# Kernel optimization log

Hardware: AMD Instinct MI355X
Metric: run time of the kernel (lower is better)

Reference implementation:

```python
import jax, jax.numpy as jnp
import numpy as np

INPUT_SIZE = 64
HIDDEN_SIZE = 256


def setup_inputs() -> dict:
    key = jax.random.key(0)
    ks = jax.random.split(key, 20)
    I, H = INPUT_SIZE, HIDDEN_SIZE
    s = 0.05
    inp = {
        "x": jax.random.normal(ks[0], (256, 512, I), jnp.float32),
        # LSTM params (PyTorch layout: [4H, in], gate order i,f,g,o)
        "w_ih": jax.random.normal(ks[1], (4 * H, I), jnp.float32) * s,
        "w_hh": jax.random.normal(ks[2], (4 * H, H), jnp.float32) * s,
        "b_ih": jax.random.normal(ks[3], (4 * H,), jnp.float32) * s,
        "b_hh": jax.random.normal(ks[4], (4 * H,), jnp.float32) * s,
        # fc_pit: H -> 64 -> 1
        "pit_w1": jax.random.normal(ks[5], (64, H), jnp.float32) * s,
        "pit_b1": jax.random.normal(ks[6], (64,), jnp.float32) * s,
        "pit_w2": jax.random.normal(ks[7], (1, 64), jnp.float32) * s,
        "pit_b2": jax.random.normal(ks[8], (1,), jnp.float32) * s,
        # fc_time: H+1 -> 64 -> 1
        "time_w1": jax.random.normal(ks[9], (64, H + 1), jnp.float32) * s,
        "time_b1": jax.random.normal(ks[10], (64,), jnp.float32) * s,
        "time_w2": jax.random.normal(ks[11], (1, 64), jnp.float32) * s,
        "time_b2": jax.random.normal(ks[12], (1,), jnp.float32) * s,
        "ar_w1": jax.random.normal(ks[13], (64, I + 2), jnp.float32) * s,
        "ar_b1": jax.random.normal(ks[14], (64,), jnp.float32) * s,
        "ar_w2": jax.random.normal(ks[15], (I, 64), jnp.float32) * s,
        "ar_b2": jax.random.normal(ks[16], (I,), jnp.float32) * s,
    }
    return inp


def _forward(x, w_ih, w_hh, b_ih, b_hh, pit_w1, pit_b1, pit_w2, pit_b2,
             time_w1, time_b1, time_w2, time_b2, ar_w1, ar_b1, ar_w2, ar_b2):
    B, S, I = x.shape
    H = w_hh.shape[1]

    def step(carry, x_orig_t):
        x_t, h, c = carry  # x_t: [B, I], h/c: [B, H]
        gates = x_t @ w_ih.T + b_ih + h @ w_hh.T + b_hh  # [B, 4H]
        i_g, f_g, g_g, o_g = jnp.split(gates, 4, axis=-1)
        i_g = jax.nn.sigmoid(i_g)
        f_g = jax.nn.sigmoid(f_g)
        g_g = jnp.tanh(g_g)
        o_g = jax.nn.sigmoid(o_g)
        c = f_g * c + i_g * g_g
        h = o_g * jnp.tanh(c)
        pit = jax.nn.relu(h @ pit_w1.T + pit_b1) @ pit_w2.T + pit_b2  # [B, 1]
        t_in = jnp.concatenate([h, pit], axis=1)  # [B, H+1]
        time = jax.nn.relu(t_in @ time_w1.T + time_b1) @ time_w2.T + time_b2  # [B, 1]
        ar_in = jnp.concatenate([pit, time, x_orig_t], axis=-1)  # [B, I+2]
        nxt = jax.nn.relu(ar_in @ ar_w1.T + ar_b1) @ ar_w2.T + ar_b2  # [B, I]
        return (nxt, h, c), (pit[:, 0], time[:, 0], nxt)

    h0 = jnp.zeros((B, H), x.dtype)
    c0 = jnp.zeros((B, H), x.dtype)
    x0 = x[:, 0, :]
    x_sbI = jnp.swapaxes(x, 0, 1)  # [S, B, I] original inputs fed at each step
    _, (pits, times, nxts) = jax.lax.scan(step, (x0, h0, c0), x_sbI)
    pit_pred = pits.T  # [B, S]
    time_pred = times.T  # [B, S]
    ar_out = jnp.concatenate([x[:, :1, :], jnp.swapaxes(nxts, 0, 1)[:, : S - 1, :]], axis=1)
    return pit_pred, time_pred, ar_out


def reference(x, w_ih, w_hh, b_ih, b_hh, pit_w1, pit_b1, pit_w2, pit_b2,
              time_w1, time_b1, time_w2, time_b2, ar_w1, ar_b1, ar_w2, ar_b2):
    return _forward(x, w_ih, w_hh, b_ih, b_hh, pit_w1, pit_b1, pit_w2, pit_b2,
                    time_w1, time_b1, time_w2, time_b2, ar_w1, ar_b1, ar_w2, ar_b2)
```

## Files before the change

kernel.cpp:

```cpp
#include <hip/hip_runtime.h>
#include <hip/hip_bf16.h>
#include <hip/hip_fp8.h>


typedef float f32x4 __attribute__((ext_vector_type(4)));
typedef short s16x8 __attribute__((ext_vector_type(8)));

#define S_LEN 512
#define I_DIM 64
#define NT    512

#define WSB_G8   0
#define WSTRIDE8 40960
#define WSB_BF   327680
#define PREP_N   368640

#define OUT_PIT  0
#define OUT_TIME 131072
#define OUT_AR   262144

#define ALD 328
#define AF8 336
#define XLD 72

__device__ __forceinline__ float sigf(float x) {
  return 1.0f / (1.0f + __expf(-x));
}
__device__ __forceinline__ float tanh_fast(float x) {
  float c = fminf(fmaxf(x, -15.0f), 15.0f);
  float e = __expf(2.0f * c);
  return (e - 1.0f) / (e + 1.0f);
}
__device__ __forceinline__ unsigned short f2bf(float f) {
  __hip_bfloat16 h = __float2bfloat16(f);
  return *reinterpret_cast<unsigned short*>(&h);
}
__device__ __forceinline__ unsigned char f2f8(float v) {
  __hip_fp8_e4m3 q(v);
  return *reinterpret_cast<unsigned char*>(&q);
}
__device__ __forceinline__ void sync_lds() {
  asm volatile("s_waitcnt lgkmcnt(0)" ::: "memory");
  __builtin_amdgcn_s_barrier();
  asm volatile("" ::: "memory");
}
__device__ __forceinline__ void gld16(const void* g, void* l) {
  __builtin_amdgcn_global_load_lds(
      (const __attribute__((address_space(1))) unsigned int*)g,
      (__attribute__((address_space(3))) unsigned int*)l, 16, 0, 0);
}

__global__ void prep_kernel(const float* __restrict__ w_ih,
                            const float* __restrict__ w_hh,
                            const float* __restrict__ pit_w1,
                            const float* __restrict__ time_w1,
                            const float* __restrict__ ar_w1,
                            const float* __restrict__ ar_w2,
                            unsigned char* __restrict__ ws8) {
  int idx = blockIdx.x * 256 + threadIdx.x;
  if (idx >= PREP_N) return;
  if (idx < WSB_G8 + 327680) {
    int w  = idx / WSTRIDE8;
    int p8 = idx - w * WSTRIDE8;
    int f  = p8 >> 9;
    int b  = p8 & 511;
    int lane = b >> 3, e = b & 7;
    int lrow = lane & 15, lgrp = lane >> 4;
    int ktidx = f >> 3, qm = f & 7;
    int kt = (ktidx < 8) ? ktidx + 2 : ktidx - 8;
    int row = (qm >> 1) * 256 + w * 32 + (qm & 1) * 16 + lrow;
    int col = kt * 32 + lgrp * 8 + e;
    float v = (col < I_DIM) ? w_ih[row * I_DIM + col]
                            : w_hh[row * 256 + col - I_DIM];
    ws8[idx] = f2f8(v);
  } else {
    int e2 = idx - 327680;
    int lane = (e2 >> 3) & 63;
    int e    = e2 & 7;
    int lrow = lane & 15, lgrp = lane >> 4;
    float v;
    if (e2 < 16384) {
      int f = e2 >> 9, wv = f >> 3, kt = f & 7;
      v = pit_w1[(wv * 16 + lrow) * 256 + kt * 32 + lgrp * 8 + e];
    } else if (e2 < 32768) {
      int f = (e2 - 16384) >> 9, wv = f >> 3, kt = f & 7;
      v = time_w1[(wv * 16 + lrow) * 257 + kt * 32 + lgrp * 8 + e];
    } else if (e2 < 36864) {
      int f = (e2 - 32768) >> 9, wv = f >> 1, kt = f & 1;
      v = ar_w1[(wv * 16 + lrow) * 66 + 2 + kt * 32 + lgrp * 8 + e];
    } else {
      int f = (e2 - 36864) >> 9, wv = f >> 1, kt = f & 1;
      v = ar_w2[(wv * 16 + lrow) * 64 + kt * 32 + lgrp * 8 + e];
    }
    ((unsigned short*)(ws8 + WSB_BF))[e2] = f2bf(v);
  }
}

#define A8FRAG(kt) (*(const long*)&A_f8[lrow][(kt) * 32 + 8 * lgrp])

#define DMA4F(ktidx, slot)                                                     \
  do {                                                                         \
    const unsigned char* g_ = wg8l + (ktidx) * 4096;                           \
    gld16(g_,        &stg8[wave][slot][0]);                                    \
    gld16(g_ + 1024, &stg8[wave][slot][1024]);                                 \
    gld16(g_ + 2048, &stg8[wave][slot][2048]);                                 \
    gld16(g_ + 3072, &stg8[wave][slot][3072]);                                 \
  } while (0)

#define GCHUNK8(af, slot)                                                      \
  do {                                                                         \
    asm volatile("s_waitcnt vmcnt(4)" ::: "memory");                           \
    _Pragma("unroll")                                                          \
    for (int s_ = 0; s_ < 8; ++s_) {                                           \
      long b_ = *(const long*)&stg8[wave][slot][s_ * 512 + lane * 8];          \
      acc2[s_] = __builtin_amdgcn_mfma_f32_16x16x32_fp8_fp8(                   \
          (af), b_, acc2[s_], 0, 0, 0);                                        \
    }                                                                          \
    asm volatile("s_waitcnt lgkmcnt(0)" ::: "memory");                         \
  } while (0)

__global__ __launch_bounds__(NT, 2) void rnn_kernel(
    const float* __restrict__ x,
    const float* __restrict__ b_ih, const float* __restrict__ b_hh,
    const float* __restrict__ pit_b1, const float* __restrict__ pit_w2,
    const float* __restrict__ pit_b2,
    const float* __restrict__ time_w1, const float* __restrict__ time_b1,
    const float* __restrict__ time_w2, const float* __restrict__ time_b2,
    const float* __restrict__ ar_w1, const float* __restrict__ ar_b1,
    const float* __restrict__ ar_b2,
    const unsigned char* __restrict__ ws8,
    float* __restrict__ out)
{
  __shared__ __align__(16) unsigned short A_lds[16][ALD];
  __shared__ __align__(16) unsigned char  A_f8[16][AF8];
  __shared__ __align__(16) unsigned short xo_lds[16][XLD];
  __shared__ __align__(16) unsigned short ar1_lds[16][XLD];
  __shared__ __align__(16) unsigned short pit_lds[32 * 512];
  __shared__ __align__(16) unsigned short tim_lds[32 * 512];
  __shared__ __align__(16) unsigned char  stg8[8][2][4096];
  __shared__ float pitp[4][16];
  __shared__ float timep[4][16];

  const int tid  = threadIdx.x;
  const int wave = tid >> 6;
  const int lane = tid & 63;
  const int lrow = lane & 15;
  const int lgrp = lane >> 4;
  const int b0   = blockIdx.x * 16;
  const int hcol = (wave & 3) * 16 + lrow;
  const unsigned char* wg8l = ws8 + wave * WSTRIDE8 + lane * 16;
  const unsigned char* wg8  = ws8 + wave * WSTRIDE8;
  const unsigned short* wsb = (const unsigned short*)(ws8 + WSB_BF);

  for (int c = tid; c < 2048; c += NT) {
    *(s16x8*)&pit_lds[c * 8] = *(const s16x8*)&wsb[c * 8];
    *(s16x8*)&tim_lds[c * 8] = *(const s16x8*)&wsb[16384 + c * 8];
  }
  for (int i = tid; i < 16 * ALD; i += NT) (&A_lds[0][0])[i] = 0;

  float gbias[8];
#pragma unroll
  for (int qm = 0; qm < 8; ++qm) {
    int g = (qm >> 1) * 256 + wave * 32 + (qm & 1) * 16 + lrow;
    gbias[qm] = b_ih[g] + b_hh[g];
  }
  s16x8 arw[2];
  float pb1v = 0, pw2v = 0, tb1v = 0, tw2v = 0, twlv = 0;
  float ab1v = 0, arpv = 0, artv = 0, ab2v = 0;
  if (wave < 4) {
    arw[0] = *(const s16x8*)&wsb[32768 + ((wave & 3) * 2 + 0) * 512 + lane * 8];
    arw[1] = *(const s16x8*)&wsb[32768 + ((wave & 3) * 2 + 1) * 512 + lane * 8];
    pb1v = pit_b1[hcol]; pw2v = pit_w2[hcol];
    ab1v = ar_b1[hcol];  arpv = ar_w1[hcol * 66]; artv = ar_w1[hcol * 66 + 1];
  } else {
    arw[0] = *(const s16x8*)&wsb[36864 + ((wave & 3) * 2 + 0) * 512 + lane * 8];
    arw[1] = *(const s16x8*)&wsb[36864 + ((wave & 3) * 2 + 1) * 512 + lane * 8];
    tb1v = time_b1[hcol]; tw2v = time_w2[hcol];
    twlv = time_w1[hcol * 257 + 256]; ab2v = ar_b2[hcol];
  }
  const float pb2 = pit_b2[0], tb2 = time_b2[0];

  const int srow = tid >> 5;
  const int sc2  = (tid & 31) * 2;
  const size_t xbase = (size_t)(b0 + srow) * S_LEN * I_DIM + sc2;
  float2 xpre = *reinterpret_cast<const float2*>(&x[xbase]);
  __syncthreads();
  A_lds[srow][sc2]     = f2bf(xpre.x);
  A_lds[srow][sc2 + 1] = f2bf(xpre.y);
  A_f8[srow][sc2]      = f2f8(xpre.x);
  A_f8[srow][sc2 + 1]  = f2f8(xpre.y);
  *reinterpret_cast<float2*>(&out[OUT_AR + xbase]) = xpre;

  float cst[2][4];
#pragma unroll
  for (int m = 0; m < 2; ++m)
#pragma unroll
    for (int r = 0; r < 4; ++r) cst[m][r] = 0.0f;
  __syncthreads();

  f32x4 acc2[8];
#pragma unroll
  for (int qm = 0; qm < 8; ++qm) {
    f32x4 tv; tv[0] = tv[1] = tv[2] = tv[3] = gbias[qm];
    acc2[qm] = tv;
  }
  {
    long a0 = A8FRAG(0);
#pragma unroll
    for (int qm = 0; qm < 8; ++qm) {
      long b = *(const long*)(wg8 + (64 + qm) * 512 + lane * 8);
      acc2[qm] = __builtin_amdgcn_mfma_f32_16x16x32_fp8_fp8(a0, b, acc2[qm], 0, 0, 0);
    }
    long a1 = A8FRAG(1);
#pragma unroll
    for (int qm = 0; qm < 8; ++qm) {
      long b = *(const long*)(wg8 + (72 + qm) * 512 + lane * 8);
      acc2[qm] = __builtin_amdgcn_mfma_f32_16x16x32_fp8_fp8(a1, b, acc2[qm], 0, 0, 0);
    }
  }
  asm volatile("s_waitcnt vmcnt(0)" ::: "memory");
  DMA4F(0, 0);
  DMA4F(1, 1);

  for (int t = 0; t < S_LEN; ++t) {
    xo_lds[srow][sc2]     = f2bf(xpre.x);
    xo_lds[srow][sc2 + 1] = f2bf(xpre.y);
    if (t + 1 < S_LEN)
      xpre = *reinterpret_cast<const float2*>(&x[xbase + (size_t)(t + 1) * I_DIM]);

#pragma unroll
    for (int m = 0; m < 2; ++m)
#pragma unroll
      for (int r = 0; r < 4; ++r) {
        float ig = sigf(acc2[0 + m][r]);
        float fg = sigf(acc2[2 + m][r]);
        float gg = tanh_fast(acc2[4 + m][r]);
        float og = sigf(acc2[6 + m][r]);
        float c  = fg * cst[m][r] + ig * gg;
        cst[m][r] = c;
        float hv = og * tanh_fast(c);
        int row = lgrp * 4 + r, col = 64 + wave * 32 + m * 16 + lrow;
        A_lds[row][col] = f2bf(hv);
        A_f8[row][col]  = f2f8(hv);
      }
#pragma unroll
    for (int qm = 0; qm < 8; ++qm) {
      f32x4 tv; tv[0] = tv[1] = tv[2] = tv[3] = gbias[qm];
      acc2[qm] = tv;
    }
    sync_lds();

    s16x8 hfr[8];
    long  hfr8[8];
#pragma unroll
    for (int k = 0; k < 8; ++k) {
      hfr[k]  = *(const s16x8*)&A_lds[lrow][64 + k * 32 + 8 * lgrp];
      hfr8[k] = *(const long*)&A_f8[lrow][64 + k * 32 + 8 * lgrp];
    }
    f32x4 hacc;
    {
      float hb = (wave < 4) ? pb1v : tb1v;
      hacc[0] = hacc[1] = hacc[2] = hacc[3] = hb;
      const unsigned short* hbp = (wave < 4) ? pit_lds : tim_lds;
#pragma unroll
      for (int kt = 0; kt < 8; ++kt) {
        s16x8 bH = *(const s16x8*)&hbp[(((wave & 3) * 8 + kt) * 64 + lane) * 8];
        hacc = __builtin_amdgcn_mfma_f32_16x16x32_bf16(hfr[kt], bH, hacc, 0, 0, 0);
      }
    }
    if (wave < 4) {
      float v[4];
#pragma unroll
      for (int r = 0; r < 4; ++r) v[r] = fmaxf(hacc[r], 0.0f) * pw2v;
#pragma unroll
      for (int off = 1; off < 16; off <<= 1)
#pragma unroll
        for (int r = 0; r < 4; ++r) v[r] += __shfl_xor(v[r], off);
      if (lrow == 0) {
#pragma unroll
        for (int r = 0; r < 4; ++r) pitp[wave][lgrp * 4 + r] = v[r];
      }
    }
    GCHUNK8(hfr8[0], 0); DMA4F(2, 0);
    GCHUNK8(hfr8[1], 1); DMA4F(3, 1);
    GCHUNK8(hfr8[2], 0); DMA4F(4, 0);
    GCHUNK8(hfr8[3], 1); DMA4F(5, 1);
    sync_lds();

    float pv[4];
#pragma unroll
    for (int r = 0; r < 4; ++r) {
      int row = lgrp * 4 + r;
      pv[r] = pitp[0][row] + pitp[1][row] + pitp[2][row] + pitp[3][row] + pb2;
    }
    f32x4 aracc;
    if (wave < 4) {
      aracc[0] = aracc[1] = aracc[2] = aracc[3] = ab1v;
#pragma unroll
      for (int kt = 0; kt < 2; ++kt) {
        s16x8 aX = *(const s16x8*)&xo_lds[lrow][kt * 32 + 8 * lgrp];
        aracc = __builtin_amdgcn_mfma_f32_16x16x32_bf16(aX, arw[kt], aracc, 0, 0, 0);
      }
      if (wave == 0 && lane < 16) {
        float pvs = pitp[0][lane] + pitp[1][lane] + pitp[2][lane] + pitp[3][lane] + pb2;
        out[OUT_PIT + (size_t)(b0 + lane) * S_LEN + t] = pvs;
      }
    } else {
      float v[4];
#pragma unroll
      for (int r = 0; r < 4; ++r)
        v[r] = fmaxf(hacc[r] + pv[r] * twlv, 0.0f) * tw2v;
#pragma unroll
      for (int off = 1; off < 16; off <<= 1)
#pragma unroll
        for (int r = 0; r < 4; ++r) v[r] += __shfl_xor(v[r], off);
      if (lrow == 0) {
#pragma unroll
        for (int r = 0; r < 4; ++r) timep[wave & 3][lgrp * 4 + r] = v[r];
      }
    }
    GCHUNK8(hfr8[4], 0); DMA4F(6, 0);
    GCHUNK8(hfr8[5], 1); DMA4F(7, 1);
    sync_lds();

    float tvv[4];
#pragma unroll
    for (int r = 0; r < 4; ++r) {
      int row = lgrp * 4 + r;
      tvv[r] = timep[0][row] + timep[1][row] + timep[2][row] + timep[3][row] + tb2;
    }
    if (wave < 4) {
#pragma unroll
      for (int r = 0; r < 4; ++r) {
        float a1 = aracc[r] + pv[r] * arpv + tvv[r] * artv;
        ar1_lds[lgrp * 4 + r][hcol] = f2bf(fmaxf(a1, 0.0f));
      }
    } else if (wave == 4 && lane < 16) {
      float tvs = timep[0][lane] + timep[1][lane] + timep[2][lane] + timep[3][lane] + tb2;
      out[OUT_TIME + (size_t)(b0 + lane) * S_LEN + t] = tvs;
    }
    GCHUNK8(hfr8[6], 0); DMA4F(8, 0);
    GCHUNK8(hfr8[7], 1); DMA4F(9, 1);
    sync_lds();

    if (wave >= 4) {
      f32x4 nacc;
      nacc[0] = nacc[1] = nacc[2] = nacc[3] = ab2v;
#pragma unroll
      for (int kt = 0; kt < 2; ++kt) {
        s16x8 aR = *(const s16x8*)&ar1_lds[lrow][kt * 32 + 8 * lgrp];
        nacc = __builtin_amdgcn_mfma_f32_16x16x32_bf16(aR, arw[kt], nacc, 0, 0, 0);
      }
#pragma unroll
      for (int r = 0; r < 4; ++r) {
        int row = lgrp * 4 + r;
        float nv = nacc[r];
        A_lds[row][hcol] = f2bf(nv);
        A_f8[row][hcol]  = f2f8(nv);
        if (t < S_LEN - 1)
          out[OUT_AR + (size_t)(b0 + row) * S_LEN * I_DIM + (size_t)(t + 1) * I_DIM + hcol] = nv;
      }
    }
    sync_lds();

    {
      long a0 = A8FRAG(0);
      GCHUNK8(a0, 0); DMA4F(0, 0);
      long a1 = A8FRAG(1);
      GCHUNK8(a1, 1); DMA4F(1, 1);
    }
  }
}

extern "C" void kernel_launch(void* const* d_in, const int* in_sizes, int n_in,
                              void* d_out, int out_size, void* d_ws, size_t ws_size,
                              hipStream_t stream) {
  const float* x       = (const float*)d_in[0];
  const float* w_ih    = (const float*)d_in[1];
  const float* w_hh    = (const float*)d_in[2];
  const float* b_ih    = (const float*)d_in[3];
  const float* b_hh    = (const float*)d_in[4];
  const float* pit_w1  = (const float*)d_in[5];
  const float* pit_b1  = (const float*)d_in[6];
  const float* pit_w2  = (const float*)d_in[7];
  const float* pit_b2  = (const float*)d_in[8];
  const float* time_w1 = (const float*)d_in[9];
  const float* time_b1 = (const float*)d_in[10];
  const float* time_w2 = (const float*)d_in[11];
  const float* time_b2 = (const float*)d_in[12];
  const float* ar_w1   = (const float*)d_in[13];
  const float* ar_b1   = (const float*)d_in[14];
  const float* ar_w2   = (const float*)d_in[15];
  const float* ar_b2   = (const float*)d_in[16];
  unsigned char* ws8   = (unsigned char*)d_ws;
  float* out           = (float*)d_out;

  prep_kernel<<<dim3((PREP_N + 255) / 256), dim3(256), 0, stream>>>(
      w_ih, w_hh, pit_w1, time_w1, ar_w1, ar_w2, ws8);
  rnn_kernel<<<dim3(16), dim3(NT), 0, stream>>>(
      x, b_ih, b_hh, pit_b1, pit_w2, pit_b2,
      time_w1, time_b1, time_w2, time_b2,
      ar_w1, ar_b1, ar_b2, ws8, out);
}
```

Measured before the change: 3.490 ms.

## Stream FC head weights as fp8 via triple-buffered DMA pipeline instead of bf16 LDS

The pit/time first-layer head weights move from bf16 copies resident in LDS to fp8 chunks stored per wave in the workspace, streamed through the same global-to-LDS DMA pipeline as the LSTM gate weights. The staging buffer grows from double to triple buffering, with adjusted vmcnt waits and a reworked half-chunk schedule for the x-input part. The bf16 copy of the activation matrix is dropped, so only the fp8 copy is written. This frees a large amount of LDS and removes bf16 stores, in exchange for more global traffic per step and lower precision in the head matmul.

Measured after the change: 3.796 ms. +8.8%, slower.

```diff
diff --git a/kernel.cpp b/kernel.cpp
--- a/kernel.cpp
+++ b/kernel.cpp
@@ -10,16 +10,14 @@
 #define I_DIM 64
 #define NT    512
 
-#define WSB_G8   0
-#define WSTRIDE8 40960
-#define WSB_BF   327680
+#define WSTRIDE8 45056
+#define WSB_BF   360448
 #define PREP_N   368640
 
 #define OUT_PIT  0
 #define OUT_TIME 131072
 #define OUT_AR   262144
 
-#define ALD 328
 #define AF8 336
 #define XLD 72
 
@@ -59,37 +57,38 @@
                             unsigned char* __restrict__ ws8) {
   int idx = blockIdx.x * 256 + threadIdx.x;
   if (idx >= PREP_N) return;
-  if (idx < WSB_G8 + 327680) {
+  if (idx < WSB_BF) {
     int w  = idx / WSTRIDE8;
     int p8 = idx - w * WSTRIDE8;
     int f  = p8 >> 9;
     int b  = p8 & 511;
     int lane = b >> 3, e = b & 7;
     int lrow = lane & 15, lgrp = lane >> 4;
-    int ktidx = f >> 3, qm = f & 7;
-    int kt = (ktidx < 8) ? ktidx + 2 : ktidx - 8;
-    int row = (qm >> 1) * 256 + w * 32 + (qm & 1) * 16 + lrow;
-    int col = kt * 32 + lgrp * 8 + e;
-    float v = (col < I_DIM) ? w_ih[row * I_DIM + col]
-                            : w_hh[row * 256 + col - I_DIM];
+    float v;
+    if (f < 8) {
+      int row = (w & 3) * 16 + lrow;
+      int col = f * 32 + lgrp * 8 + e;
+      v = (w < 4) ? pit_w1[row * 256 + col] : time_w1[row * 257 + col];
+    } else {
+      int g = f - 8;
+      int ktidx = g >> 3, qm = g & 7;
+      int kt = (ktidx < 8) ? ktidx + 2 : ktidx - 8;
+      int row = (qm >> 1) * 256 + w * 32 + (qm & 1) * 16 + lrow;
+      int col = kt * 32 + lgrp * 8 + e;
+      v = (col < I_DIM) ? w_ih[row * I_DIM + col] : w_hh[row * 256 + col - I_DIM];
+    }
     ws8[idx] = f2f8(v);
   } else {
-    int e2 = idx - 327680;
+    int e2 = idx - WSB_BF;
     int lane = (e2 >> 3) & 63;
     int e    = e2 & 7;
     int lrow = lane & 15, lgrp = lane >> 4;
     float v;
-    if (e2 < 16384) {
-      int f = e2 >> 9, wv = f >> 3, kt = f & 7;
-      v = pit_w1[(wv * 16 + lrow) * 256 + kt * 32 + lgrp * 8 + e];
-    } else if (e2 < 32768) {
-      int f = (e2 - 16384) >> 9, wv = f >> 3, kt = f & 7;
-      v = time_w1[(wv * 16 + lrow) * 257 + kt * 32 + lgrp * 8 + e];
-    } else if (e2 < 36864) {
-      int f = (e2 - 32768) >> 9, wv = f >> 1, kt = f & 1;
+    if (e2 < 4096) {
+      int f = e2 >> 9, wv = f >> 1, kt = f & 1;
       v = ar_w1[(wv * 16 + lrow) * 66 + 2 + kt * 32 + lgrp * 8 + e];
     } else {
-      int f = (e2 - 36864) >> 9, wv = f >> 1, kt = f & 1;
+      int f = (e2 - 4096) >> 9, wv = f >> 1, kt = f & 1;
       v = ar_w2[(wv * 16 + lrow) * 64 + kt * 32 + lgrp * 8 + e];
     }
     ((unsigned short*)(ws8 + WSB_BF))[e2] = f2bf(v);
@@ -98,23 +97,51 @@
 
 #define A8FRAG(kt) (*(const long*)&A_f8[lrow][(kt) * 32 + 8 * lgrp])
 
-#define DMA4F(ktidx, slot)                                                     \
+#define DMA4F(byteoff, slot)                                                   \
   do {                                                                         \
-    const unsigned char* g_ = wg8l + (ktidx) * 4096;                           \
+    const unsigned char* g_ = wg8l + (byteoff);                                \
     gld16(g_,        &stg8[wave][slot][0]);                                    \
     gld16(g_ + 1024, &stg8[wave][slot][1024]);                                 \
     gld16(g_ + 2048, &stg8[wave][slot][2048]);                                 \
     gld16(g_ + 3072, &stg8[wave][slot][3072]);                                 \
   } while (0)
-
-#define GCHUNK8(af, slot)                                                      \
+#define DMA2F(byteoff, slot)                                                   \
   do {                                                                         \
-    asm volatile("s_waitcnt vmcnt(4)" ::: "memory");                           \
+    const unsigned char* g_ = wg8l + (byteoff);                                \
+    gld16(g_,        &stg8[wave][slot][0]);                                    \
+    gld16(g_ + 1024, &stg8[wave][slot][1024]);                                 \
+  } while (0)
+
+#define CHEADF(slot, N)                                                        \
+  do {                                                                         \
+    asm volatile("s_waitcnt vmcnt(" #N ")" ::: "memory");                      \
+    _Pragma("unroll")                                                          \
+    for (int k_ = 0; k_ < 8; ++k_) {                                           \
+      long b_ = *(const long*)&stg8[wave][slot][k_ * 512 + lane * 8];          \
+      hacc = __builtin_amdgcn_mfma_f32_16x16x32_fp8_fp8(hfr8[k_], b_,          \
+                                                        hacc, 0, 0, 0);        \
+    }                                                                          \
+    asm volatile("s_waitcnt lgkmcnt(0)" ::: "memory");                         \
+  } while (0)
+#define GCHUNK8(af, slot, N)                                                   \
+  do {                                                                         \
+    asm volatile("s_waitcnt vmcnt(" #N ")" ::: "memory");                      \
     _Pragma("unroll")                                                          \
     for (int s_ = 0; s_ < 8; ++s_) {                                           \
       long b_ = *(const long*)&stg8[wave][slot][s_ * 512 + lane * 8];          \
       acc2[s_] = __builtin_amdgcn_mfma_f32_16x16x32_fp8_fp8(                   \
           (af), b_, acc2[s_], 0, 0, 0);                                        \
+    }                                                                          \
+    asm volatile("s_waitcnt lgkmcnt(0)" ::: "memory");                         \
+  } while (0)
+#define GHALF4(af, slot, N, qb)                                                \
+  do {                                                                         \
+    asm volatile("s_waitcnt vmcnt(" #N ")" ::: "memory");                      \
+    _Pragma("unroll")                                                          \
+    for (int s_ = 0; s_ < 4; ++s_) {                                           \
+      long b_ = *(const long*)&stg8[wave][slot][s_ * 512 + lane * 8];          \
+      acc2[(qb) + s_] = __builtin_amdgcn_mfma_f32_16x16x32_fp8_fp8(            \
+          (af), b_, acc2[(qb) + s_], 0, 0, 0);                                 \
     }                                                                          \
     asm volatile("s_waitcnt lgkmcnt(0)" ::: "memory");                         \
   } while (0)
@@ -131,13 +158,10 @@
     const unsigned char* __restrict__ ws8,
     float* __restrict__ out)
 {
-  __shared__ __align__(16) unsigned short A_lds[16][ALD];
   __shared__ __align__(16) unsigned char  A_f8[16][AF8];
   __shared__ __align__(16) unsigned short xo_lds[16][XLD];
   __shared__ __align__(16) unsigned short ar1_lds[16][XLD];
-  __shared__ __align__(16) unsigned short pit_lds[32 * 512];
-  __shared__ __align__(16) unsigned short tim_lds[32 * 512];
-  __shared__ __align__(16) unsigned char  stg8[8][2][4096];
+  __shared__ __align__(16) unsigned char  stg8[8][3][4096];
   __shared__ float pitp[4][16];
   __shared__ float timep[4][16];
 
@@ -152,11 +176,7 @@
   const unsigned char* wg8  = ws8 + wave * WSTRIDE8;
   const unsigned short* wsb = (const unsigned short*)(ws8 + WSB_BF);
 
-  for (int c = tid; c < 2048; c += NT) {
-    *(s16x8*)&pit_lds[c * 8] = *(const s16x8*)&wsb[c * 8];
-    *(s16x8*)&tim_lds[c * 8] = *(const s16x8*)&wsb[16384 + c * 8];
-  }
-  for (int i = tid; i < 16 * ALD; i += NT) (&A_lds[0][0])[i] = 0;
+  for (int i = tid; i < 16 * AF8; i += NT) (&A_f8[0][0])[i] = 0;
 
   float gbias[8];
 #pragma unroll
@@ -168,13 +188,13 @@
   float pb1v = 0, pw2v = 0, tb1v = 0, tw2v = 0, twlv = 0;
   float ab1v = 0, arpv = 0, artv = 0, ab2v = 0;
   if (wave < 4) {
-    arw[0] = *(const s16x8*)&wsb[32768 + ((wave & 3) * 2 + 0) * 512 + lane * 8];
-    arw[1] = *(const s16x8*)&wsb[32768 + ((wave & 3) * 2 + 1) * 512 + lane * 8];
+    arw[0] = *(const s16x8*)&wsb[((wave & 3) * 2 + 0) * 512 + lane * 8];
+    arw[1] = *(const s16x8*)&wsb[((wave & 3) * 2 + 1) * 512 + lane * 8];
     pb1v = pit_b1[hcol]; pw2v = pit_w2[hcol];
     ab1v = ar_b1[hcol];  arpv = ar_w1[hcol * 66]; artv = ar_w1[hcol * 66 + 1];
   } else {
-    arw[0] = *(const s16x8*)&wsb[36864 + ((wave & 3) * 2 + 0) * 512 + lane * 8];
-    arw[1] = *(const s16x8*)&wsb[36864 + ((wave & 3) * 2 + 1) * 512 + lane * 8];
+    arw[0] = *(const s16x8*)&wsb[4096 + ((wave & 3) * 2 + 0) * 512 + lane * 8];
+    arw[1] = *(const s16x8*)&wsb[4096 + ((wave & 3) * 2 + 1) * 512 + lane * 8];
     tb1v = time_b1[hcol]; tw2v = time_w2[hcol];
     twlv = time_w1[hcol * 257 + 256]; ab2v = ar_b2[hcol];
   }
@@ -185,10 +205,8 @@
   const size_t xbase = (size_t)(b0 + srow) * S_LEN * I_DIM + sc2;
   float2 xpre = *reinterpret_cast<const float2*>(&x[xbase]);
   __syncthreads();
-  A_lds[srow][sc2]     = f2bf(xpre.x);
-  A_lds[srow][sc2 + 1] = f2bf(xpre.y);
-  A_f8[srow][sc2]      = f2f8(xpre.x);
-  A_f8[srow][sc2 + 1]  = f2f8(xpre.y);
+  A_f8[srow][sc2]     = f2f8(xpre.x);
+  A_f8[srow][sc2 + 1] = f2f8(xpre.y);
   *reinterpret_cast<float2*>(&out[OUT_AR + xbase]) = xpre;
 
   float cst[2][4];
@@ -208,19 +226,20 @@
     long a0 = A8FRAG(0);
 #pragma unroll
     for (int qm = 0; qm < 8; ++qm) {
-      long b = *(const long*)(wg8 + (64 + qm) * 512 + lane * 8);
+      long b = *(const long*)(wg8 + 36864 + qm * 512 + lane * 8);
       acc2[qm] = __builtin_amdgcn_mfma_f32_16x16x32_fp8_fp8(a0, b, acc2[qm], 0, 0, 0);
     }
     long a1 = A8FRAG(1);
 #pragma unroll
     for (int qm = 0; qm < 8; ++qm) {
-      long b = *(const long*)(wg8 + (72 + qm) * 512 + lane * 8);
+      long b = *(const long*)(wg8 + 40960 + qm * 512 + lane * 8);
       acc2[qm] = __builtin_amdgcn_mfma_f32_16x16x32_fp8_fp8(a1, b, acc2[qm], 0, 0, 0);
     }
   }
   asm volatile("s_waitcnt vmcnt(0)" ::: "memory");
   DMA4F(0, 0);
-  DMA4F(1, 1);
+  DMA4F(4096, 1);
+  DMA4F(8192, 2);
 
   for (int t = 0; t < S_LEN; ++t) {
     xo_lds[srow][sc2]     = f2bf(xpre.x);
@@ -238,10 +257,7 @@
         float og = sigf(acc2[6 + m][r]);
         float c  = fg * cst[m][r] + ig * gg;
         cst[m][r] = c;
-        float hv = og * tanh_fast(c);
-        int row = lgrp * 4 + r, col = 64 + wave * 32 + m * 16 + lrow;
-        A_lds[row][col] = f2bf(hv);
-        A_f8[row][col]  = f2f8(hv);
+        A_f8[lgrp * 4 + r][64 + wave * 32 + m * 16 + lrow] = f2f8(og * tanh_fast(c));
       }
 #pragma unroll
     for (int qm = 0; qm < 8; ++qm) {
@@ -250,24 +266,20 @@
     }
     sync_lds();
 
-    s16x8 hfr[8];
-    long  hfr8[8];
-#pragma unroll
-    for (int k = 0; k < 8; ++k) {
-      hfr[k]  = *(const s16x8*)&A_lds[lrow][64 + k * 32 + 8 * lgrp];
+    long hfr8[8];
+#pragma unroll
+    for (int k = 0; k < 8; ++k)
       hfr8[k] = *(const long*)&A_f8[lrow][64 + k * 32 + 8 * lgrp];
-    }
+
     f32x4 hacc;
     {
       float hb = (wave < 4) ? pb1v : tb1v;
       hacc[0] = hacc[1] = hacc[2] = hacc[3] = hb;
-      const unsigned short* hbp = (wave < 4) ? pit_lds : tim_lds;
-#pragma unroll
-      for (int kt = 0; kt < 8; ++kt) {
-        s16x8 bH = *(const s16x8*)&hbp[(((wave & 3) * 8 + kt) * 64 + lane) * 8];
-        hacc = __builtin_amdgcn_mfma_f32_16x16x32_bf16(hfr[kt], bH, hacc, 0, 0, 0);
-      }
-    }
+    }
+    CHEADF(0, 8);            DMA4F(12288, 0);
+    GCHUNK8(hfr8[0], 1, 8);  DMA4F(16384, 1);
+    GCHUNK8(hfr8[1], 2, 8);  DMA4F(20480, 2);
+
     if (wave < 4) {
       float v[4];
 #pragma unroll
@@ -281,10 +293,8 @@
         for (int r = 0; r < 4; ++r) pitp[wave][lgrp * 4 + r] = v[r];
       }
     }
-    GCHUNK8(hfr8[0], 0); DMA4F(2, 0);
-    GCHUNK8(hfr8[1], 1); DMA4F(3, 1);
-    GCHUNK8(hfr8[2], 0); DMA4F(4, 0);
-    GCHUNK8(hfr8[3], 1); DMA4F(5, 1);
+    GCHUNK8(hfr8[2], 0, 8);  DMA4F(24576, 0);
+    GCHUNK8(hfr8[3], 1, 8);  DMA4F(28672, 1);
     sync_lds();
 
     float pv[4];
@@ -319,8 +329,8 @@
         for (int r = 0; r < 4; ++r) timep[wave & 3][lgrp * 4 + r] = v[r];
       }
     }
-    GCHUNK8(hfr8[4], 0); DMA4F(6, 0);
-    GCHUNK8(hfr8[5], 1); DMA4F(7, 1);
+    GCHUNK8(hfr8[4], 2, 8);  DMA4F(32768, 2);
+    GCHUNK8(hfr8[5], 0, 8);  DMA4F(36864, 0);
     sync_lds();
 
     float tvv[4];
@@ -339,8 +349,8 @@
       float tvs = timep[0][lane] + timep[1][lane] + timep[2][lane] + timep[3][lane] + tb2;
       out[OUT_TIME + (size_t)(b0 + lane) * S_LEN + t] = tvs;
     }
-    GCHUNK8(hfr8[6], 0); DMA4F(8, 0);
-    GCHUNK8(hfr8[7], 1); DMA4F(9, 1);
+    GCHUNK8(hfr8[6], 1, 8);  DMA2F(40960, 1);
+    GCHUNK8(hfr8[7], 2, 6);  DMA2F(43008, 2);
     sync_lds();
 
     if (wave >= 4) {
@@ -355,8 +365,7 @@
       for (int r = 0; r < 4; ++r) {
         int row = lgrp * 4 + r;
         float nv = nacc[r];
-        A_lds[row][hcol] = f2bf(nv);
-        A_f8[row][hcol]  = f2f8(nv);
+        A_f8[row][hcol] = f2f8(nv);
         if (t < S_LEN - 1)
           out[OUT_AR + (size_t)(b0 + row) * S_LEN * I_DIM + (size_t)(t + 1) * I_DIM + hcol] = nv;
       }
@@ -365,9 +374,10 @@
 
     {
       long a0 = A8FRAG(0);
-      GCHUNK8(a0, 0); DMA4F(0, 0);
+      GCHUNK8(a0, 0, 4);     DMA4F(0, 0);
       long a1 = A8FRAG(1);
-      GCHUNK8(a1, 1); DMA4F(1, 1);
+      GHALF4(a1, 1, 6, 0);   DMA4F(4096, 1);
+      GHALF4(a1, 2, 8, 4);   DMA4F(8192, 2);
     }
   }
 }
```

## Double workgroup to 16 waves, split gate columns and head roles across waves

Applied to the files above, without the earlier changes.

Raises the block from 8 to 16 waves so that each wave owns 16 hidden columns (4 gate accumulators) instead of 32, halving the per-wave fp8 weight streaming and MFMA chain on the recurrent critical path. The pit, time, AR-first-layer and AR-second-layer heads are now assigned to disjoint groups of four waves rather than sharing waves. Launch bounds drop from 2 blocks per CU to 1, and the per-step barriers now synchronise twice as many waves, which costs occupancy and adds sync overhead.

After: 4.549 ms. +30.3%, slower.

```diff
diff --git a/kernel.cpp b/kernel.cpp
--- a/kernel.cpp
+++ b/kernel.cpp
@@ -8,10 +8,9 @@
 
 #define S_LEN 512
 #define I_DIM 64
-#define NT    512
-
-#define WSB_G8   0
-#define WSTRIDE8 40960
+#define NT    1024
+
+#define WSTRIDE8 20480
 #define WSB_BF   327680
 #define PREP_N   368640
 
@@ -59,22 +58,22 @@
                             unsigned char* __restrict__ ws8) {
   int idx = blockIdx.x * 256 + threadIdx.x;
   if (idx >= PREP_N) return;
-  if (idx < WSB_G8 + 327680) {
+  if (idx < WSB_BF) {
     int w  = idx / WSTRIDE8;
     int p8 = idx - w * WSTRIDE8;
     int f  = p8 >> 9;
     int b  = p8 & 511;
     int lane = b >> 3, e = b & 7;
     int lrow = lane & 15, lgrp = lane >> 4;
-    int ktidx = f >> 3, qm = f & 7;
+    int ktidx = f >> 2, q = f & 3;
     int kt = (ktidx < 8) ? ktidx + 2 : ktidx - 8;
-    int row = (qm >> 1) * 256 + w * 32 + (qm & 1) * 16 + lrow;
+    int row = q * 256 + w * 16 + lrow;
     int col = kt * 32 + lgrp * 8 + e;
     float v = (col < I_DIM) ? w_ih[row * I_DIM + col]
                             : w_hh[row * 256 + col - I_DIM];
     ws8[idx] = f2f8(v);
   } else {
-    int e2 = idx - 327680;
+    int e2 = idx - WSB_BF;
     int lane = (e2 >> 3) & 63;
     int e    = e2 & 7;
     int lrow = lane & 15, lgrp = lane >> 4;
@@ -98,28 +97,26 @@
 
 #define A8FRAG(kt) (*(const long*)&A_f8[lrow][(kt) * 32 + 8 * lgrp])
 
-#define DMA4F(ktidx, slot)                                                     \
+#define DMAC(byteoff, slot)                                                    \
   do {                                                                         \
-    const unsigned char* g_ = wg8l + (ktidx) * 4096;                           \
+    const unsigned char* g_ = wg8l + (byteoff);                                \
     gld16(g_,        &stg8[wave][slot][0]);                                    \
     gld16(g_ + 1024, &stg8[wave][slot][1024]);                                 \
-    gld16(g_ + 2048, &stg8[wave][slot][2048]);                                 \
-    gld16(g_ + 3072, &stg8[wave][slot][3072]);                                 \
   } while (0)
 
-#define GCHUNK8(af, slot)                                                      \
+#define GCHUNK(af, slot)                                                       \
   do {                                                                         \
-    asm volatile("s_waitcnt vmcnt(4)" ::: "memory");                           \
+    asm volatile("s_waitcnt vmcnt(2)" ::: "memory");                           \
     _Pragma("unroll")                                                          \
-    for (int s_ = 0; s_ < 8; ++s_) {                                           \
-      long b_ = *(const long*)&stg8[wave][slot][s_ * 512 + lane * 8];          \
-      acc2[s_] = __builtin_amdgcn_mfma_f32_16x16x32_fp8_fp8(                   \
-          (af), b_, acc2[s_], 0, 0, 0);                                        \
+    for (int q_ = 0; q_ < 4; ++q_) {                                           \
+      long b_ = *(const long*)&stg8[wave][slot][q_ * 512 + lane * 8];          \
+      acc2[q_] = __builtin_amdgcn_mfma_f32_16x16x32_fp8_fp8(                   \
+          (af), b_, acc2[q_], 0, 0, 0);                                        \
     }                                                                          \
     asm volatile("s_waitcnt lgkmcnt(0)" ::: "memory");                         \
   } while (0)
 
-__global__ __launch_bounds__(NT, 2) void rnn_kernel(
+__global__ __launch_bounds__(NT, 1) void rnn_kernel(
     const float* __restrict__ x,
     const float* __restrict__ b_ih, const float* __restrict__ b_hh,
     const float* __restrict__ pit_b1, const float* __restrict__ pit_w2,
@@ -137,7 +134,7 @@
   __shared__ __align__(16) unsigned short ar1_lds[16][XLD];
   __shared__ __align__(16) unsigned short pit_lds[32 * 512];
   __shared__ __align__(16) unsigned short tim_lds[32 * 512];
-  __shared__ __align__(16) unsigned char  stg8[8][2][4096];
+  __shared__ __align__(16) unsigned char  stg8[16][2][2048];
   __shared__ float pitp[4][16];
   __shared__ float timep[4][16];
 
@@ -157,115 +154,114 @@
     *(s16x8*)&tim_lds[c * 8] = *(const s16x8*)&wsb[16384 + c * 8];
   }
   for (int i = tid; i < 16 * ALD; i += NT) (&A_lds[0][0])[i] = 0;
-
-  float gbias[8];
-#pragma unroll
-  for (int qm = 0; qm < 8; ++qm) {
-    int g = (qm >> 1) * 256 + wave * 32 + (qm & 1) * 16 + lrow;
-    gbias[qm] = b_ih[g] + b_hh[g];
-  }
+  for (int i = tid; i < 16 * AF8; i += NT) (&A_f8[0][0])[i] = 0;
+
+  float gbias[4];
+#pragma unroll
+  for (int q = 0; q < 4; ++q)
+    gbias[q] = b_ih[q * 256 + wave * 16 + lrow] + b_hh[q * 256 + wave * 16 + lrow];
+
   s16x8 arw[2];
   float pb1v = 0, pw2v = 0, tb1v = 0, tw2v = 0, twlv = 0;
   float ab1v = 0, arpv = 0, artv = 0, ab2v = 0;
   if (wave < 4) {
+    pb1v = pit_b1[hcol]; pw2v = pit_w2[hcol];
+  } else if (wave < 8) {
+    tb1v = time_b1[hcol]; tw2v = time_w2[hcol];
+    twlv = time_w1[hcol * 257 + 256];
+  } else if (wave < 12) {
     arw[0] = *(const s16x8*)&wsb[32768 + ((wave & 3) * 2 + 0) * 512 + lane * 8];
     arw[1] = *(const s16x8*)&wsb[32768 + ((wave & 3) * 2 + 1) * 512 + lane * 8];
-    pb1v = pit_b1[hcol]; pw2v = pit_w2[hcol];
-    ab1v = ar_b1[hcol];  arpv = ar_w1[hcol * 66]; artv = ar_w1[hcol * 66 + 1];
+    ab1v = ar_b1[hcol]; arpv = ar_w1[hcol * 66]; artv = ar_w1[hcol * 66 + 1];
   } else {
     arw[0] = *(const s16x8*)&wsb[36864 + ((wave & 3) * 2 + 0) * 512 + lane * 8];
     arw[1] = *(const s16x8*)&wsb[36864 + ((wave & 3) * 2 + 1) * 512 + lane * 8];
-    tb1v = time_b1[hcol]; tw2v = time_w2[hcol];
-    twlv = time_w1[hcol * 257 + 256]; ab2v = ar_b2[hcol];
+    ab2v = ar_b2[hcol];
   }
   const float pb2 = pit_b2[0], tb2 = time_b2[0];
 
-  const int srow = tid >> 5;
-  const int sc2  = (tid & 31) * 2;
-  const size_t xbase = (size_t)(b0 + srow) * S_LEN * I_DIM + sc2;
-  float2 xpre = *reinterpret_cast<const float2*>(&x[xbase]);
+  const int srow = tid >> 6;
+  const int scol = tid & 63;
+  const size_t xbase = (size_t)(b0 + srow) * S_LEN * I_DIM + scol;
+  float xpre = x[xbase];
   __syncthreads();
-  A_lds[srow][sc2]     = f2bf(xpre.x);
-  A_lds[srow][sc2 + 1] = f2bf(xpre.y);
-  A_f8[srow][sc2]      = f2f8(xpre.x);
-  A_f8[srow][sc2 + 1]  = f2f8(xpre.y);
-  *reinterpret_cast<float2*>(&out[OUT_AR + xbase]) = xpre;
-
-  float cst[2][4];
-#pragma unroll
-  for (int m = 0; m < 2; ++m)
-#pragma unroll
-    for (int r = 0; r < 4; ++r) cst[m][r] = 0.0f;
+  A_lds[srow][scol] = f2bf(xpre);
+  A_f8[srow][scol]  = f2f8(xpre);
+  out[OUT_AR + xbase] = xpre;
+
+  float cst[4] = {0.0f, 0.0f, 0.0f, 0.0f};
   __syncthreads();
 
-  f32x4 acc2[8];
-#pragma unroll
-  for (int qm = 0; qm < 8; ++qm) {
-    f32x4 tv; tv[0] = tv[1] = tv[2] = tv[3] = gbias[qm];
-    acc2[qm] = tv;
+  f32x4 acc2[4];
+#pragma unroll
+  for (int q = 0; q < 4; ++q) {
+    f32x4 tv; tv[0] = tv[1] = tv[2] = tv[3] = gbias[q];
+    acc2[q] = tv;
   }
   {
     long a0 = A8FRAG(0);
 #pragma unroll
-    for (int qm = 0; qm < 8; ++qm) {
-      long b = *(const long*)(wg8 + (64 + qm) * 512 + lane * 8);
-      acc2[qm] = __builtin_amdgcn_mfma_f32_16x16x32_fp8_fp8(a0, b, acc2[qm], 0, 0, 0);
+    for (int q = 0; q < 4; ++q) {
+      long b = *(const long*)(wg8 + (32 + q) * 512 + lane * 8);
+      acc2[q] = __builtin_amdgcn_mfma_f32_16x16x32_fp8_fp8(a0, b, acc2[q], 0, 0, 0);
     }
     long a1 = A8FRAG(1);
 #pragma unroll
-    for (int qm = 0; qm < 8; ++qm) {
-      long b = *(const long*)(wg8 + (72 + qm) * 512 + lane * 8);
-      acc2[qm] = __builtin_amdgcn_mfma_f32_16x16x32_fp8_fp8(a1, b, acc2[qm], 0, 0, 0);
+    for (int q = 0; q < 4; ++q) {
+      long b = *(const long*)(wg8 + (36 + q) * 512 + lane * 8);
+      acc2[q] = __builtin_amdgcn_mfma_f32_16x16x32_fp8_fp8(a1, b, acc2[q], 0, 0, 0);
     }
   }
   asm volatile("s_waitcnt vmcnt(0)" ::: "memory");
-  DMA4F(0, 0);
-  DMA4F(1, 1);
+  DMAC(0, 0);
+  DMAC(2048, 1);
 
   for (int t = 0; t < S_LEN; ++t) {
-    xo_lds[srow][sc2]     = f2bf(xpre.x);
-    xo_lds[srow][sc2 + 1] = f2bf(xpre.y);
-    if (t + 1 < S_LEN)
-      xpre = *reinterpret_cast<const float2*>(&x[xbase + (size_t)(t + 1) * I_DIM]);
-
-#pragma unroll
-    for (int m = 0; m < 2; ++m)
-#pragma unroll
-      for (int r = 0; r < 4; ++r) {
-        float ig = sigf(acc2[0 + m][r]);
-        float fg = sigf(acc2[2 + m][r]);
-        float gg = tanh_fast(acc2[4 + m][r]);
-        float og = sigf(acc2[6 + m][r]);
-        float c  = fg * cst[m][r] + ig * gg;
-        cst[m][r] = c;
-        float hv = og * tanh_fast(c);
-        int row = lgrp * 4 + r, col = 64 + wave * 32 + m * 16 + lrow;
-        A_lds[row][col] = f2bf(hv);
-        A_f8[row][col]  = f2f8(hv);
-      }
-#pragma unroll
-    for (int qm = 0; qm < 8; ++qm) {
-      f32x4 tv; tv[0] = tv[1] = tv[2] = tv[3] = gbias[qm];
-      acc2[qm] = tv;
-    }
-    sync_lds();
-
-    s16x8 hfr[8];
-    long  hfr8[8];
-#pragma unroll
-    for (int k = 0; k < 8; ++k) {
-      hfr[k]  = *(const s16x8*)&A_lds[lrow][64 + k * 32 + 8 * lgrp];
+    xo_lds[srow][scol] = f2bf(xpre);
+    if (t + 1 < S_LEN) xpre = x[xbase + (size_t)(t + 1) * I_DIM];
+
+#pragma unroll
+    for (int r = 0; r < 4; ++r) {
+      float ig = sigf(acc2[0][r]);
+      float fg = sigf(acc2[1][r]);
+      float gg = tanh_fast(acc2[2][r]);
+      float og = sigf(acc2[3][r]);
+      float c  = fg * cst[r] + ig * gg;
+      cst[r] = c;
+      float hv = og * tanh_fast(c);
+      int row = lgrp * 4 + r, col = 64 + wave * 16 + lrow;
+      A_lds[row][col] = f2bf(hv);
+      A_f8[row][col]  = f2f8(hv);
+    }
+#pragma unroll
+    for (int q = 0; q < 4; ++q) {
+      f32x4 tv; tv[0] = tv[1] = tv[2] = tv[3] = gbias[q];
+      acc2[q] = tv;
+    }
+    sync_lds();
+
+    long hfr8[8];
+#pragma unroll
+    for (int k = 0; k < 8; ++k)
       hfr8[k] = *(const long*)&A_f8[lrow][64 + k * 32 + 8 * lgrp];
-    }
-    f32x4 hacc;
-    {
+
+    f32x4 hacc, aracc;
+    if (wave < 8) {
       float hb = (wave < 4) ? pb1v : tb1v;
       hacc[0] = hacc[1] = hacc[2] = hacc[3] = hb;
       const unsigned short* hbp = (wave < 4) ? pit_lds : tim_lds;
 #pragma unroll
       for (int kt = 0; kt < 8; ++kt) {
-        s16x8 bH = *(const s16x8*)&hbp[(((wave & 3) * 8 + kt) * 64 + lane) * 8];
-        hacc = __builtin_amdgcn_mfma_f32_16x16x32_bf16(hfr[kt], bH, hacc, 0, 0, 0);
+        s16x8 aH = *(const s16x8*)&A_lds[lrow][64 + kt * 32 + 8 * lgrp];
+        s16x8 bH = *(const s16x8*)&hbp[((wave & 3) * 8 + kt) * 512 + lane * 8];
+        hacc = __builtin_amdgcn_mfma_f32_16x16x32_bf16(aH, bH, hacc, 0, 0, 0);
+      }
+    } else if (wave < 12) {
+      aracc[0] = aracc[1] = aracc[2] = aracc[3] = ab1v;
+#pragma unroll
+      for (int kt = 0; kt < 2; ++kt) {
+        s16x8 aX = *(const s16x8*)&xo_lds[lrow][kt * 32 + 8 * lgrp];
+        aracc = __builtin_amdgcn_mfma_f32_16x16x32_bf16(aX, arw[kt], aracc, 0, 0, 0);
       }
     }
     if (wave < 4) {
@@ -281,10 +277,10 @@
         for (int r = 0; r < 4; ++r) pitp[wave][lgrp * 4 + r] = v[r];
       }
     }
-    GCHUNK8(hfr8[0], 0); DMA4F(2, 0);
-    GCHUNK8(hfr8[1], 1); DMA4F(3, 1);
-    GCHUNK8(hfr8[2], 0); DMA4F(4, 0);
-    GCHUNK8(hfr8[3], 1); DMA4F(5, 1);
+    GCHUNK(hfr8[0], 0); DMAC(4096, 0);
+    GCHUNK(hfr8[1], 1); DMAC(6144, 1);
+    GCHUNK(hfr8[2], 0); DMAC(8192, 0);
+    GCHUNK(hfr8[3], 1); DMAC(10240, 1);
     sync_lds();
 
     float pv[4];
@@ -293,19 +289,7 @@
       int row = lgrp * 4 + r;
       pv[r] = pitp[0][row] + pitp[1][row] + pitp[2][row] + pitp[3][row] + pb2;
     }
-    f32x4 aracc;
-    if (wave < 4) {
-      aracc[0] = aracc[1] = aracc[2] = aracc[3] = ab1v;
-#pragma unroll
-      for (int kt = 0; kt < 2; ++kt) {
-        s16x8 aX = *(const s16x8*)&xo_lds[lrow][kt * 32 + 8 * lgrp];
-        aracc = __builtin_amdgcn_mfma_f32_16x16x32_bf16(aX, arw[kt], aracc, 0, 0, 0);
-      }
-      if (wave == 0 && lane < 16) {
-        float pvs = pitp[0][lane] + pitp[1][lane] + pitp[2][lane] + pitp[3][lane] + pb2;
-        out[OUT_PIT + (size_t)(b0 + lane) * S_LEN + t] = pvs;
-      }
-    } else {
+    if (wave >= 4 && wave < 8) {
       float v[4];
 #pragma unroll
       for (int r = 0; r < 4; ++r)
@@ -318,9 +302,12 @@
 #pragma unroll
         for (int r = 0; r < 4; ++r) timep[wave & 3][lgrp * 4 + r] = v[r];
       }
-    }
-    GCHUNK8(hfr8[4], 0); DMA4F(6, 0);
-    GCHUNK8(hfr8[5], 1); DMA4F(7, 1);
+    } else if (wave == 0 && lane < 16) {
+      float pvs = pitp[0][lane] + pitp[1][lane] + pitp[2][lane] + pitp[3][lane] + pb2;
+      out[OUT_PIT + (size_t)(b0 + lane) * S_LEN + t] = pvs;
+    }
+    GCHUNK(hfr8[4], 0); DMAC(12288, 0);
+    GCHUNK(hfr8[5], 1); DMAC(14336, 1);
     sync_lds();
 
     float tvv[4];
@@ -329,7 +316,7 @@
       int row = lgrp * 4 + r;
       tvv[r] = timep[0][row] + timep[1][row] + timep[2][row] + timep[3][row] + tb2;
     }
-    if (wave < 4) {
+    if (wave >= 8 && wave < 12) {
 #pragma unroll
       for (int r = 0; r < 4; ++r) {
         float a1 = aracc[r] + pv[r] * arpv + tvv[r] * artv;
@@ -339,11 +326,11 @@
       float tvs = timep[0][lane] + timep[1][lane] + timep[2][lane] + timep[3][lane] + tb2;
       out[OUT_TIME + (size_t)(b0 + lane) * S_LEN + t] = tvs;
     }
-    GCHUNK8(hfr8[6], 0); DMA4F(8, 0);
-    GCHUNK8(hfr8[7], 1); DMA4F(9, 1);
-    sync_lds();
-
-    if (wave >= 4) {
+    GCHUNK(hfr8[6], 0); DMAC(16384, 0);
+    GCHUNK(hfr8[7], 1); DMAC(18432, 1);
+    sync_lds();
+
+    if (wave >= 12) {
       f32x4 nacc;
       nacc[0] = nacc[1] = nacc[2] = nacc[3] = ab2v;
 #pragma unroll
@@ -365,9 +352,9 @@
 
     {
       long a0 = A8FRAG(0);
-      GCHUNK8(a0, 0); DMA4F(0, 0);
+      GCHUNK(a0, 0); DMAC(0, 0);
       long a1 = A8FRAG(1);
-      GCHUNK8(a1, 1); DMA4F(1, 1);
+      GCHUNK(a1, 1); DMAC(2048, 1);
     }
   }
 }
```
